# Kernel tuning notes

Hardware: AMD Instinct MI355X
Metric: run time of the kernel (lower is better)

Reference implementation:

```python
import jax, jax.numpy as jnp
import numpy as np

TOP_K = 8


def setup_inputs() -> dict:
    key = jax.random.key(0)
    k1, k2 = jax.random.split(key)
    hidden_states = jax.random.normal(k1, (4, 4096, 4096), dtype=jnp.float32)
    weight = jax.random.normal(k2, (64, 4096), dtype=jnp.float32) * 0.02
    return {"hidden_states": hidden_states, "weight": weight}


def reference(hidden_states, weight):
    # Flatten [B, S, H] -> [T, H]; gating math is done in float32 (matches .float()).
    h = hidden_states.shape[-1]
    x = hidden_states.reshape(-1, h).astype(jnp.float32)
    # Router logits: [T, E] = [T, H] @ [H, E]
    logits = jnp.einsum('th,eh->te', x, weight.astype(jnp.float32))
    scores = jax.nn.softmax(logits, axis=-1)
    # Top-k expert selection (greedy router)
    topk_weight, topk_idx = jax.lax.top_k(scores, TOP_K)  # [T, K], [T, K]
    # Normalize top-k probabilities (norm_topk_prob=True)
    denom = jnp.sum(topk_weight, axis=-1, keepdims=True) + 1e-20
    topk_weight = topk_weight / denom
    return topk_weight, topk_idx
```

## Files before the change

### kernel.cpp

```cpp
#include <hip/hip_runtime.h>
#include <math.h>

typedef float  f32x4  __attribute__((ext_vector_type(4)));
typedef int    i32x4  __attribute__((ext_vector_type(4)));

#define H      4096
#define E      64
#define TOPK   8
#define TILE_T 32
#define CK     256
#define MS     4
#define NCH    16

__global__ __launch_bounds__(256)
void prep_w(const float* __restrict__ Wg, signed char* __restrict__ Wb)
{
  int n = blockIdx.x * 256 + threadIdx.x;
  int kgrp = n & 3, m = (n >> 2) & 63, e = n >> 8;
  const float* wp = Wg + e * 4096 + m * 64 + kgrp * 16;
  signed char lb[5][16];
  #pragma unroll
  for (int s = 0; s < 16; ++s) {
    long long v = (long long)rint((double)wp[s] * 2199023255552.0);
    #pragma unroll
    for (int j = 0; j < 4; ++j) {
      signed char b = (signed char)(v & 0xff);
      lb[j][s] = b;
      v = (v - b) >> 8;
    }
    lb[4][s] = (signed char)v;
  }
  int lanei = (kgrp << 4) | (e & 15);
  int eq = e >> 4;
  #pragma unroll
  for (int j = 0; j < 5; ++j) {
    i32x4 d;
    #pragma unroll
    for (int r = 0; r < 4; ++r)
      d[r] = (lb[j][4*r] & 0xFF) | ((lb[j][4*r+1] & 0xFF) << 8)
           | ((lb[j][4*r+2] & 0xFF) << 16) | ((lb[j][4*r+3] & 0xFF) << 24);
    *(i32x4*)(Wb + (((size_t)(m * 4 + eq) * 5 + j) << 10) + lanei * 16) = d;
  }
}

__global__ __launch_bounds__(64)
void comp_w(const float* __restrict__ Wg, double* __restrict__ compT)
{
  int e = blockIdx.x;
  int lane = threadIdx.x;
  double s = 0.0;
  #pragma unroll 4
  for (int i = 0; i < 64; ++i)
    s += rint((double)Wg[e * 4096 + i * 64 + lane] * 2199023255552.0);
  #pragma unroll
  for (int off = 32; off >= 1; off >>= 1)
    s += __shfl_xor(s, off);
  if (lane == 0) compT[e] = 8421504.0 * s;
}

__global__ __launch_bounds__(256)
void moe_gate_i8(const float* __restrict__ X, const signed char* __restrict__ Wb,
                 const double* __restrict__ compT, float* __restrict__ out,
                 int n_tokens)
{
  __shared__ char sm[32768];
  double* Ls = (double*)sm;

  const int tid  = threadIdx.x;
  const int lane = tid & 63;
  const int w    = tid >> 6;
  const int t0   = blockIdx.x * TILE_T;
  const int l15  = lane & 15;
  const int kg   = lane >> 4;

  i32x4 z = {0, 0, 0, 0};
  int lab = l15 * 0x01010101;
  i32x4 onev = {0x01010101, 0x01010101, 0x01010101, 0x01010101};
  i32x4 labv = {lab, lab, lab, lab};
  i32x4 pr = __builtin_amdgcn_mfma_i32_16x16x64_i8(labv, onev, z, 0, 0, 0);
  i32x4 pc = __builtin_amdgcn_mfma_i32_16x16x64_i8(onev, labv, z, 0, 0, 0);
  int qrow[4], qcol[4];
  #pragma unroll
  for (int r = 0; r < 4; ++r) { qrow[r] = pr[r] >> 6; qcol[r] = pc[r] >> 6; }

  i32x4 aA3 = z, aA4 = z, aA5 = z, aA6 = z, aA7 = z;
  i32x4 aB3 = z, aB4 = z, aB5 = z, aB6 = z, aB7 = z;

  const int tt = tid >> 3;
  const int ks = tid & 7;
  const float* xp = X + (size_t)(t0 + tt) * H + ks * 32;

  const signed char* bpp = Wb + w * 5120 + lane * 16;

  for (int c = 0; c < NCH; ++c) {
    f32x4 xr[8];
    #pragma unroll
    for (int q = 0; q < 8; ++q) xr[q] = *(const f32x4*)(xp + 4 * q);
    xp += CK;

    #pragma unroll
    for (int hf = 0; hf < 2; ++hf) {
      unsigned w32[16];
      #pragma unroll
      for (int r = 0; r < 4; ++r) {
        f32x4 xv = xr[hf * 4 + r];
        #pragma unroll
        for (int jj = 0; jj < 4; ++jj)
          w32[r*4+jj] = ((unsigned)(int)(xv[jj] * 268435456.0f)) ^ 0x00808080u;
      }
      i32x4 W0, W1, W2, W3;
      #pragma unroll
      for (int r = 0; r < 4; ++r) {
        unsigned u0 = w32[4*r], u1 = w32[4*r+1], u2 = w32[4*r+2], u3 = w32[4*r+3];
        unsigned p01, p23;
        p01 = __builtin_amdgcn_perm(u1, u0, 0x04000400u);
        p23 = __builtin_amdgcn_perm(u3, u2, 0x04000400u);
        W0[r] = (int)__builtin_amdgcn_perm(p23, p01, 0x05040100u);
        p01 = __builtin_amdgcn_perm(u1, u0, 0x05010501u);
        p23 = __builtin_amdgcn_perm(u3, u2, 0x05010501u);
        W1[r] = (int)__builtin_amdgcn_perm(p23, p01, 0x05040100u);
        p01 = __builtin_amdgcn_perm(u1, u0, 0x06020602u);
        p23 = __builtin_amdgcn_perm(u3, u2, 0x06020602u);
        W2[r] = (int)__builtin_amdgcn_perm(p23, p01, 0x05040100u);
        p01 = __builtin_amdgcn_perm(u1, u0, 0x07030703u);
        p23 = __builtin_amdgcn_perm(u3, u2, 0x07030703u);
        W3[r] = (int)__builtin_amdgcn_perm(p23, p01, 0x05040100u);
      }
      const int kgrp = ks * 2 + hf;
      const int swzw = ks << 4;
      char* base = sm + (kgrp << 11) + (((tt << 4) ^ swzw));
      *(i32x4*)(base + 0x000) = W0;
      *(i32x4*)(base + 0x200) = W1;
      *(i32x4*)(base + 0x400) = W2;
      *(i32x4*)(base + 0x600) = W3;
    }
    __syncthreads();

    #pragma unroll
    for (int m = 0; m < MS; ++m) {
      const int kq   = 4 * m + kg;
      const int swzr = ((kq >> 1) & 7) << 4;
      const char* abase = sm + (kq << 11) + (((l15 << 4) ^ swzr));
      i32x4 b0 = *(const i32x4*)(bpp);
      i32x4 b1 = *(const i32x4*)(bpp + 1024);
      i32x4 b2 = *(const i32x4*)(bpp + 2048);
      i32x4 b3 = *(const i32x4*)(bpp + 3072);
      i32x4 b4 = *(const i32x4*)(bpp + 4096);
      bpp += 20480;
      i32x4 xA0 = *(const i32x4*)(abase + 0x000);
      i32x4 xA1 = *(const i32x4*)(abase + 0x200);
      i32x4 xA2 = *(const i32x4*)(abase + 0x400);
      i32x4 xA3 = *(const i32x4*)(abase + 0x600);
      i32x4 xB0 = *(const i32x4*)(abase + 0x100);
      i32x4 xB1 = *(const i32x4*)(abase + 0x300);
      i32x4 xB2 = *(const i32x4*)(abase + 0x500);
      i32x4 xB3 = *(const i32x4*)(abase + 0x700);
      aA3 = __builtin_amdgcn_mfma_i32_16x16x64_i8(xA0, b3, aA3, 0, 0, 0);
      aB3 = __builtin_amdgcn_mfma_i32_16x16x64_i8(xB0, b3, aB3, 0, 0, 0);
      aA4 = __builtin_amdgcn_mfma_i32_16x16x64_i8(xA0, b4, aA4, 0, 0, 0);
      aB4 = __builtin_amdgcn_mfma_i32_16x16x64_i8(xB0, b4, aB4, 0, 0, 0);
      aA5 = __builtin_amdgcn_mfma_i32_16x16x64_i8(xA1, b4, aA5, 0, 0, 0);
      aB5 = __builtin_amdgcn_mfma_i32_16x16x64_i8(xB1, b4, aB5, 0, 0, 0);
      aA6 = __builtin_amdgcn_mfma_i32_16x16x64_i8(xA2, b4, aA6, 0, 0, 0);
      aB6 = __builtin_amdgcn_mfma_i32_16x16x64_i8(xB2, b4, aB6, 0, 0, 0);
      aA7 = __builtin_amdgcn_mfma_i32_16x16x64_i8(xA3, b4, aA7, 0, 0, 0);
      aB7 = __builtin_amdgcn_mfma_i32_16x16x64_i8(xB3, b4, aB7, 0, 0, 0);
      aA3 = __builtin_amdgcn_mfma_i32_16x16x64_i8(xA1, b2, aA3, 0, 0, 0);
      aB3 = __builtin_amdgcn_mfma_i32_16x16x64_i8(xB1, b2, aB3, 0, 0, 0);
      aA4 = __builtin_amdgcn_mfma_i32_16x16x64_i8(xA1, b3, aA4, 0, 0, 0);
      aB4 = __builtin_amdgcn_mfma_i32_16x16x64_i8(xB1, b3, aB4, 0, 0, 0);
      aA5 = __builtin_amdgcn_mfma_i32_16x16x64_i8(xA2, b3, aA5, 0, 0, 0);
      aB5 = __builtin_amdgcn_mfma_i32_16x16x64_i8(xB2, b3, aB5, 0, 0, 0);
      aA6 = __builtin_amdgcn_mfma_i32_16x16x64_i8(xA3, b3, aA6, 0, 0, 0);
      aB6 = __builtin_amdgcn_mfma_i32_16x16x64_i8(xB3, b3, aB6, 0, 0, 0);
      aA3 = __builtin_amdgcn_mfma_i32_16x16x64_i8(xA2, b1, aA3, 0, 0, 0);
      aB3 = __builtin_amdgcn_mfma_i32_16x16x64_i8(xB2, b1, aB3, 0, 0, 0);
      aA4 = __builtin_amdgcn_mfma_i32_16x16x64_i8(xA2, b2, aA4, 0, 0, 0);
      aB4 = __builtin_amdgcn_mfma_i32_16x16x64_i8(xB2, b2, aB4, 0, 0, 0);
      aA5 = __builtin_amdgcn_mfma_i32_16x16x64_i8(xA3, b2, aA5, 0, 0, 0);
      aB5 = __builtin_amdgcn_mfma_i32_16x16x64_i8(xB3, b2, aB5, 0, 0, 0);
      aA3 = __builtin_amdgcn_mfma_i32_16x16x64_i8(xA3, b0, aA3, 0, 0, 0);
      aB3 = __builtin_amdgcn_mfma_i32_16x16x64_i8(xB3, b0, aB3, 0, 0, 0);
      aA4 = __builtin_amdgcn_mfma_i32_16x16x64_i8(xA3, b1, aA4, 0, 0, 0);
      aB4 = __builtin_amdgcn_mfma_i32_16x16x64_i8(xB3, b1, aB4, 0, 0, 0);
    }
    __syncthreads();
  }

  #pragma unroll
  for (int r = 0; r < 4; ++r) {
    int ex = w * 16 + qcol[r];
    double pA = (16777216.0          * (double)aA3[r]
               + 4294967296.0        * (double)aA4[r]
               + 1099511627776.0     * (double)aA5[r]
               + 281474976710656.0   * (double)aA6[r]
               + 72057594037927936.0 * (double)aA7[r]
               + compT[ex]) * 1.6940658945086007e-21;
    double pB = (16777216.0          * (double)aB3[r]
               + 4294967296.0        * (double)aB4[r]
               + 1099511627776.0     * (double)aB5[r]
               + 281474976710656.0   * (double)aB6[r]
               + 72057594037927936.0 * (double)aB7[r]
               + compT[ex]) * 1.6940658945086007e-21;
    Ls[qrow[r] * E + ex]        = pA;
    Ls[(16 + qrow[r]) * E + ex] = pB;
  }
  __syncthreads();

  for (int tt2 = 0; tt2 < 8; tt2++) {
    int t = w * 8 + tt2;
    double val = Ls[t * E + lane];

    double mx = val;
    #pragma unroll
    for (int off = 32; off >= 1; off >>= 1)
      mx = fmax(mx, __shfl_xor(mx, off));

    float p = expf((float)(val - mx));
    float S = p;
    #pragma unroll
    for (int off = 32; off >= 1; off >>= 1)
      S += __shfl_xor(S, off);

    double cur = val;
    float myw = 0.f; int myidx = 0;
    float psum = 0.f;
    #pragma unroll
    for (int r = 0; r < TOPK; r++) {
      double v = cur; int ii = lane;
      #pragma unroll
      for (int off = 32; off >= 1; off >>= 1) {
        double ov = __shfl_xor(v, off);
        int    oi = __shfl_xor(ii, off);
        if (ov > v || (ov == v && oi < ii)) { v = ov; ii = oi; }
      }
      float pw = __shfl(p, ii);
      psum += pw;
      if (lane == r) { myw = pw; myidx = ii; }
      if (lane == ii) cur = -INFINITY;
    }
    float denom = psum + 1e-20f * S;
    if (lane < TOPK) {
      size_t gt = (size_t)(t0 + t);
      out[gt * TOPK + lane] = myw / denom;
      out[(size_t)n_tokens * TOPK + gt * TOPK + lane] = (float)myidx;
    }
  }
}

extern "C" void kernel_launch(void* const* d_in, const int* in_sizes, int n_in,
                              void* d_out, int out_size, void* d_ws, size_t ws_size,
                              hipStream_t stream)
{
  const float* X  = (const float*)d_in[0];
  const float* Wg = (const float*)d_in[1];
  float* out = (float*)d_out;
  signed char* Wb = (signed char*)d_ws;
  double* compT   = (double*)((char*)d_ws + 1310720);
  int n_tokens = in_sizes[0] / H;

  prep_w<<<64, 256, 0, stream>>>(Wg, Wb);
  comp_w<<<64, 64, 0, stream>>>(Wg, compT);
  moe_gate_i8<<<n_tokens / TILE_T, 256, 0, stream>>>(X, Wb, compT, out, n_tokens);
}
```

Before: 141.3 us.

## Software-pipeline X chunk loads and conversion behind MFMA compute

Adds a prologue that stages the first X chunk in shared memory, then in each iteration issues global loads for the next chunk before running the MFMAs on the current one, converting and storing afterward. This is meant to hide global-memory latency of the activation stream behind int8 matrix work. It also requests two blocks per CU via launch bounds, which constrains registers and may cause spills given the extra live registers held across the MFMA loop.

```diff
diff --git a/kernel.cpp b/kernel.cpp
--- a/kernel.cpp
+++ b/kernel.cpp
@@ -58,7 +58,7 @@
   if (lane == 0) compT[e] = 8421504.0 * s;
 }
 
-__global__ __launch_bounds__(256)
+__global__ __launch_bounds__(256, 2)
 void moe_gate_i8(const float* __restrict__ X, const signed char* __restrict__ Wb,
                  const double* __restrict__ compT, float* __restrict__ out,
                  int n_tokens)
@@ -88,53 +88,67 @@
 
   const int tt = tid >> 3;
   const int ks = tid & 7;
+  const int kgrpw = ks * 2;
+  const int swzw  = ks << 4;
+  char* wbase0 = sm + ((kgrpw + 0) << 11) + (((tt << 4) ^ swzw));
+  char* wbase1 = sm + ((kgrpw + 1) << 11) + (((tt << 4) ^ swzw));
   const float* xp = X + (size_t)(t0 + tt) * H + ks * 32;
 
   const signed char* bpp = Wb + w * 5120 + lane * 16;
+
+  #define CONV(xr, hf, W0, W1, W2, W3)                                        \
+  {                                                                           \
+    unsigned w32[16];                                                         \
+    _Pragma("unroll")                                                         \
+    for (int r = 0; r < 4; ++r) {                                             \
+      f32x4 xv = xr[(hf) * 4 + r];                                            \
+      _Pragma("unroll")                                                       \
+      for (int jj = 0; jj < 4; ++jj)                                          \
+        w32[r*4+jj] = ((unsigned)(int)(xv[jj] * 268435456.0f)) ^ 0x00808080u; \
+    }                                                                         \
+    _Pragma("unroll")                                                         \
+    for (int r = 0; r < 4; ++r) {                                             \
+      unsigned u0 = w32[4*r], u1 = w32[4*r+1], u2 = w32[4*r+2], u3 = w32[4*r+3];\
+      unsigned p01, p23;                                                      \
+      p01 = __builtin_amdgcn_perm(u1, u0, 0x04000400u);                       \
+      p23 = __builtin_amdgcn_perm(u3, u2, 0x04000400u);                       \
+      W0[r] = (int)__builtin_amdgcn_perm(p23, p01, 0x05040100u);              \
+      p01 = __builtin_amdgcn_perm(u1, u0, 0x05010501u);                       \
+      p23 = __builtin_amdgcn_perm(u3, u2, 0x05010501u);                       \
+      W1[r] = (int)__builtin_amdgcn_perm(p23, p01, 0x05040100u);              \
+      p01 = __builtin_amdgcn_perm(u1, u0, 0x06020602u);                       \
+      p23 = __builtin_amdgcn_perm(u3, u2, 0x06020602u);                       \
+      W2[r] = (int)__builtin_amdgcn_perm(p23, p01, 0x05040100u);              \
+      p01 = __builtin_amdgcn_perm(u1, u0, 0x07030703u);                       \
+      p23 = __builtin_amdgcn_perm(u3, u2, 0x07030703u);                       \
+      W3[r] = (int)__builtin_amdgcn_perm(p23, p01, 0x05040100u);              \
+    }                                                                         \
+  }
+
+  {
+    f32x4 xr[8];
+    #pragma unroll
+    for (int q = 0; q < 8; ++q) xr[q] = *(const f32x4*)(xp + 4 * q);
+    xp += CK;
+    i32x4 U0, U1, U2, U3, V0, V1, V2, V3;
+    CONV(xr, 0, U0, U1, U2, U3);
+    CONV(xr, 1, V0, V1, V2, V3);
+    *(i32x4*)(wbase0 + 0x000) = U0;
+    *(i32x4*)(wbase0 + 0x200) = U1;
+    *(i32x4*)(wbase0 + 0x400) = U2;
+    *(i32x4*)(wbase0 + 0x600) = U3;
+    *(i32x4*)(wbase1 + 0x000) = V0;
+    *(i32x4*)(wbase1 + 0x200) = V1;
+    *(i32x4*)(wbase1 + 0x400) = V2;
+    *(i32x4*)(wbase1 + 0x600) = V3;
+  }
+  __syncthreads();
 
   for (int c = 0; c < NCH; ++c) {
     f32x4 xr[8];
     #pragma unroll
     for (int q = 0; q < 8; ++q) xr[q] = *(const f32x4*)(xp + 4 * q);
-    xp += CK;
-
-    #pragma unroll
-    for (int hf = 0; hf < 2; ++hf) {
-      unsigned w32[16];
-      #pragma unroll
-      for (int r = 0; r < 4; ++r) {
-        f32x4 xv = xr[hf * 4 + r];
-        #pragma unroll
-        for (int jj = 0; jj < 4; ++jj)
-          w32[r*4+jj] = ((unsigned)(int)(xv[jj] * 268435456.0f)) ^ 0x00808080u;
-      }
-      i32x4 W0, W1, W2, W3;
-      #pragma unroll
-      for (int r = 0; r < 4; ++r) {
-        unsigned u0 = w32[4*r], u1 = w32[4*r+1], u2 = w32[4*r+2], u3 = w32[4*r+3];
-        unsigned p01, p23;
-        p01 = __builtin_amdgcn_perm(u1, u0, 0x04000400u);
-        p23 = __builtin_amdgcn_perm(u3, u2, 0x04000400u);
-        W0[r] = (int)__builtin_amdgcn_perm(p23, p01, 0x05040100u);
-        p01 = __builtin_amdgcn_perm(u1, u0, 0x05010501u);
-        p23 = __builtin_amdgcn_perm(u3, u2, 0x05010501u);
-        W1[r] = (int)__builtin_amdgcn_perm(p23, p01, 0x05040100u);
-        p01 = __builtin_amdgcn_perm(u1, u0, 0x06020602u);
-        p23 = __builtin_amdgcn_perm(u3, u2, 0x06020602u);
-        W2[r] = (int)__builtin_amdgcn_perm(p23, p01, 0x05040100u);
-        p01 = __builtin_amdgcn_perm(u1, u0, 0x07030703u);
-        p23 = __builtin_amdgcn_perm(u3, u2, 0x07030703u);
-        W3[r] = (int)__builtin_amdgcn_perm(p23, p01, 0x05040100u);
-      }
-      const int kgrp = ks * 2 + hf;
-      const int swzw = ks << 4;
-      char* base = sm + (kgrp << 11) + (((tt << 4) ^ swzw));
-      *(i32x4*)(base + 0x000) = W0;
-      *(i32x4*)(base + 0x200) = W1;
-      *(i32x4*)(base + 0x400) = W2;
-      *(i32x4*)(base + 0x600) = W3;
-    }
-    __syncthreads();
+    xp += (c < NCH - 2) ? CK : 0;
 
     #pragma unroll
     for (int m = 0; m < MS; ++m) {
@@ -184,8 +198,23 @@
       aA4 = __builtin_amdgcn_mfma_i32_16x16x64_i8(xA3, b1, aA4, 0, 0, 0);
       aB4 = __builtin_amdgcn_mfma_i32_16x16x64_i8(xB3, b1, aB4, 0, 0, 0);
     }
+
+    i32x4 U0, U1, U2, U3, V0, V1, V2, V3;
+    CONV(xr, 0, U0, U1, U2, U3);
+    CONV(xr, 1, V0, V1, V2, V3);
+
     __syncthreads();
-  }
+    *(i32x4*)(wbase0 + 0x000) = U0;
+    *(i32x4*)(wbase0 + 0x200) = U1;
+    *(i32x4*)(wbase0 + 0x400) = U2;
+    *(i32x4*)(wbase0 + 0x600) = U3;
+    *(i32x4*)(wbase1 + 0x000) = V0;
+    *(i32x4*)(wbase1 + 0x200) = V1;
+    *(i32x4*)(wbase1 + 0x400) = V2;
+    *(i32x4*)(wbase1 + 0x600) = V3;
+    __syncthreads();
+  }
+  #undef CONV
 
   #pragma unroll
   for (int r = 0; r < 4; ++r) {
```

New measurement: 183.1 us. 29.6% more time.
